# Kernel tuning notes

Measured on AMD Instinct MI355X. Metric: run time of the kernel, lower is better.

Reference implementation:

```python
import jax, jax.numpy as jnp
import numpy as np

B, C, H, W = 8, 256, 64, 64
CQK = C // 8


def setup_inputs() -> dict:
    key = jax.random.key(0)
    ks = jax.random.split(key, 9)
    s_in = 1.0 / np.sqrt(C)
    return {
        "feature1": jax.random.normal(ks[0], (B, C, H, W), jnp.float32),
        "feature2": jax.random.normal(ks[1], (B, C, H, W), jnp.float32),
        "feature3": jax.random.normal(ks[2], (B, C, H, W), jnp.float32),
        # 1x1 conv weights stored as [out_ch, in_ch]
        "wq": jax.random.uniform(ks[3], (CQK, C), jnp.float32, -s_in, s_in),
        "bq": jax.random.uniform(ks[4], (CQK,), jnp.float32, -s_in, s_in),
        "wk": jax.random.uniform(ks[5], (CQK, C), jnp.float32, -s_in, s_in),
        "bk": jax.random.uniform(ks[6], (CQK,), jnp.float32, -s_in, s_in),
        "wv": jax.random.uniform(ks[7], (C, C), jnp.float32, -s_in, s_in),
        "bv": jax.random.uniform(ks[8], (C,), jnp.float32, -s_in, s_in),
    }


def reference(feature1, feature2, feature3, wq, bq, wk, bk, wv, bv):
    b, c, h, w = feature1.shape
    hw = h * w
    # 1x1 convs == per-pixel channel GEMMs
    q = jnp.einsum('bchw,oc->bohw', feature1, wq) + bq[None, :, None, None]
    k = jnp.einsum('bchw,oc->bohw', feature2, wk) + bk[None, :, None, None]
    v = jnp.einsum('bchw,oc->bohw', feature3, wv) + bv[None, :, None, None]
    q = q.reshape(b, -1, hw).transpose(0, 2, 1)  # [b, hw, cqk]
    k = k.reshape(b, -1, hw)                      # [b, cqk, hw]
    v = v.reshape(b, -1, hw)                      # [b, c, hw]
    attn = jax.nn.softmax(jnp.einsum('bnc,bcm->bnm', q, k), axis=-1)  # [b, hw, hw]
    # fused = value @ attn^T  -> [b, c, hw]
    fused = jnp.einsum('bcm,bnm->bcn', v, attn)
    return fused.reshape(b, c, h, w)
```

## Files before the change

### kernel.cpp

```cpp
#include <hip/hip_runtime.h>
#include <math.h>

#define BATCH 8
#define CH    256
#define HWPIX 4096
#define CQK_  32

typedef __bf16 bf16x8 __attribute__((ext_vector_type(8)));
typedef __bf16 bf16x4 __attribute__((ext_vector_type(4)));
typedef __bf16 bf16x2 __attribute__((ext_vector_type(2)));
typedef float  f32x4  __attribute__((ext_vector_type(4)));

#define FS_STR 68

static __device__ inline bf16x8 ld_frag(const __bf16* p) {
  bf16x4 lo = *(const bf16x4*)p;
  bf16x4 hi = *(const bf16x4*)(p + 4);
  return __builtin_shufflevector(lo, hi, 0, 1, 2, 3, 4, 5, 6, 7);
}

static __device__ inline bf16x8 w_frag(const float* p) {
  const float4 a = *(const float4*)p;
  const float4 b = *(const float4*)(p + 4);
  bf16x8 r;
  r[0] = (__bf16)a.x; r[1] = (__bf16)a.y; r[2] = (__bf16)a.z; r[3] = (__bf16)a.w;
  r[4] = (__bf16)b.x; r[5] = (__bf16)b.y; r[6] = (__bf16)b.z; r[7] = (__bf16)b.w;
  return r;
}

__global__ __launch_bounds__(256) void proj_qk_mfma(
    const float* __restrict__ f, const float* __restrict__ W,
    const float* __restrict__ bias, __bf16* __restrict__ outT)
{
  __shared__ __align__(16) __bf16 f_s[64 * FS_STR];
  const int t    = threadIdx.x;
  const int w    = __builtin_amdgcn_readfirstlane(t >> 6);
  const int lane = t & 63;
  const int q16  = lane & 15;
  const int quad = lane >> 4;
  const int b    = blockIdx.y;
  const int n0   = blockIdx.x * 64;
  const float* fb = f + (size_t)b * CH * HWPIX + n0;

  const float bo0 = bias[q16];
  const float bo1 = bias[16 + q16];

  f32x4 acc[2];
  acc[0] = (f32x4){0.f, 0.f, 0.f, 0.f};
  acc[1] = (f32x4){0.f, 0.f, 0.f, 0.f};

  for (int c0 = 0; c0 < CH; c0 += 64) {
    {
      const int n  = t & 63;
      const int cp = (t >> 6) * 2;
#pragma unroll
      for (int k = 0; k < 8; ++k) {
        const int cin = cp + k * 8;
        bf16x2 pk;
        pk[0] = (__bf16)fb[(size_t)(c0 + cin) * HWPIX + n];
        pk[1] = (__bf16)fb[(size_t)(c0 + cin + 1) * HWPIX + n];
        *(bf16x2*)&f_s[n * FS_STR + cin] = pk;
      }
    }
    __syncthreads();

    bf16x8 af[2];
#pragma unroll
    for (int kh = 0; kh < 2; ++kh)
      af[kh] = ld_frag(&f_s[(16 * w + q16) * FS_STR + 32 * kh + quad * 8]);

#pragma unroll
    for (int ot = 0; ot < 2; ++ot) {
#pragma unroll
      for (int kh = 0; kh < 2; ++kh) {
        const bf16x8 wf =
            w_frag(W + (size_t)(16 * ot + q16) * CH + c0 + 32 * kh + quad * 8);
        acc[ot] = __builtin_amdgcn_mfma_f32_16x16x32_bf16(af[kh], wf, acc[ot], 0, 0, 0);
      }
    }
    __syncthreads();
  }

#pragma unroll
  for (int r = 0; r < 4; ++r) {
    const size_t row = (size_t)b * HWPIX + n0 + 16 * w + quad * 4 + r;
    outT[row * CQK_ + q16]      = (__bf16)(acc[0][r] + bo0);
    outT[row * CQK_ + 16 + q16] = (__bf16)(acc[1][r] + bo1);
  }
}

__global__ __launch_bounds__(256) void proj_v_mfma(
    const float* __restrict__ f, const float* __restrict__ W,
    const float* __restrict__ bias, __bf16* __restrict__ outv)
{
  __shared__ __align__(16) __bf16 f_s[64 * FS_STR];
  const int t     = threadIdx.x;
  const int w     = __builtin_amdgcn_readfirstlane(t >> 6);
  const int lane  = t & 63;
  const int q16   = lane & 15;
  const int quad  = lane >> 4;
  const int b     = blockIdx.z;
  const int n0    = blockIdx.x * 64;
  const int cbase = blockIdx.y * 64;
  const float* fb = f + (size_t)b * CH * HWPIX + n0;
  const int crow  = cbase + 16 * w + q16;

  f32x4 acc[4];
#pragma unroll
  for (int nt = 0; nt < 4; ++nt) acc[nt] = (f32x4){0.f, 0.f, 0.f, 0.f};

  for (int c0 = 0; c0 < CH; c0 += 64) {
    {
      const int n  = t & 63;
      const int cp = (t >> 6) * 2;
#pragma unroll
      for (int k = 0; k < 8; ++k) {
        const int cin = cp + k * 8;
        bf16x2 pk;
        pk[0] = (__bf16)fb[(size_t)(c0 + cin) * HWPIX + n];
        pk[1] = (__bf16)fb[(size_t)(c0 + cin + 1) * HWPIX + n];
        *(bf16x2*)&f_s[n * FS_STR + cin] = pk;
      }
    }
    __syncthreads();

    bf16x8 af[2];
#pragma unroll
    for (int kh = 0; kh < 2; ++kh)
      af[kh] = w_frag(W + (size_t)crow * CH + c0 + 32 * kh + quad * 8);

#pragma unroll
    for (int nt = 0; nt < 4; ++nt) {
#pragma unroll
      for (int kh = 0; kh < 2; ++kh) {
        const bf16x8 bfr = ld_frag(&f_s[(16 * nt + q16) * FS_STR + 32 * kh + quad * 8]);
        acc[nt] = __builtin_amdgcn_mfma_f32_16x16x32_bf16(af[kh], bfr, acc[nt], 0, 0, 0);
      }
    }
    __syncthreads();
  }

  const float4 bi = *(const float4*)&bias[cbase + 16 * w + quad * 4];
#pragma unroll
  for (int nt = 0; nt < 4; ++nt) {
#pragma unroll
    for (int r = 0; r < 4; ++r) {
      const int c = cbase + 16 * w + quad * 4 + r;
      outv[((size_t)b * CH + c) * HWPIX + n0 + 16 * nt + q16] =
          (__bf16)(acc[nt][r] + ((const float*)&bi)[r]);
    }
  }
}

__global__ __launch_bounds__(256, 2) void attn_kernel(
    const __bf16* __restrict__ qT, const __bf16* __restrict__ kT,
    const __bf16* __restrict__ vv, float* __restrict__ out)
{
  __shared__ __align__(16) __bf16 p_s[64 * 72];
  __shared__ float L_s[64];

  const int t    = threadIdx.x;
  const int w    = __builtin_amdgcn_readfirstlane(t >> 6);
  const int lane = t & 63;
  const int q16  = lane & 15;
  const int quad = lane >> 4;

  const int b  = blockIdx.x & 7;
  const int q0 = (blockIdx.x >> 3) * 64;

  const __bf16* kTb = kT + (size_t)b * HWPIX * CQK_;
  const __bf16* vbp = vv + ((size_t)b * CH + 64 * w) * HWPIX;

  const bf16x8 qfrag =
      *(const bf16x8*)(qT + ((size_t)b * HWPIX + q0 + 16 * w + q16) * CQK_ + quad * 8);

  f32x4 oacc[4][4];
#pragma unroll
  for (int i = 0; i < 4; ++i)
#pragma unroll
    for (int j = 0; j < 4; ++j)
      oacc[i][j] = (f32x4){0.f, 0.f, 0.f, 0.f};
  float Lp[4] = {0.f, 0.f, 0.f, 0.f};

  bf16x8 kf[4];
#pragma unroll
  for (int mt = 0; mt < 4; ++mt)
    kf[mt] = *(const bf16x8*)(kTb + (size_t)(16 * mt + q16) * CQK_ + quad * 8);

  for (int m0 = 0; m0 < HWPIX; m0 += 64) {
    f32x4 S[4];
#pragma unroll
    for (int mt = 0; mt < 4; ++mt)
      S[mt] = __builtin_amdgcn_mfma_f32_16x16x32_bf16(
          qfrag, kf[mt], (f32x4){0.f, 0.f, 0.f, 0.f}, 0, 0, 0);

    bf16x8 vf[4][2];
#pragma unroll
    for (int ct = 0; ct < 4; ++ct)
#pragma unroll
      for (int mh = 0; mh < 2; ++mh)
        vf[ct][mh] = *(const bf16x8*)(vbp + (size_t)(16 * ct + q16) * HWPIX
                                      + m0 + 32 * mh + quad * 8);

#pragma unroll
    for (int mt = 0; mt < 4; ++mt) {
#pragma unroll
      for (int r = 0; r < 4; ++r) {
        const float e = __expf(S[mt][r]);
        Lp[r] += e;
        p_s[(16 * w + quad * 4 + r) * 72 + 16 * mt + q16] = (__bf16)e;
      }
    }
    __syncthreads();

    const int mn = (m0 + 64) & (HWPIX - 1);
#pragma unroll
    for (int mt = 0; mt < 4; ++mt)
      kf[mt] = *(const bf16x8*)(kTb + (size_t)(mn + 16 * mt + q16) * CQK_ + quad * 8);

    bf16x8 pf[4][2];
#pragma unroll
    for (int nt = 0; nt < 4; ++nt)
#pragma unroll
      for (int mh = 0; mh < 2; ++mh)
        pf[nt][mh] = *(const bf16x8*)(&p_s[(16 * nt + q16) * 72 + 32 * mh + quad * 8]);

#pragma unroll
    for (int ct = 0; ct < 4; ++ct)
#pragma unroll
      for (int nt = 0; nt < 4; ++nt)
#pragma unroll
        for (int mh = 0; mh < 2; ++mh)
          oacc[ct][nt] = __builtin_amdgcn_mfma_f32_16x16x32_bf16(
              vf[ct][mh], pf[nt][mh], oacc[ct][nt], 0, 0, 0);
    __syncthreads();
  }

#pragma unroll
  for (int r = 0; r < 4; ++r) {
    Lp[r] += __shfl_xor(Lp[r], 1);
    Lp[r] += __shfl_xor(Lp[r], 2);
    Lp[r] += __shfl_xor(Lp[r], 4);
    Lp[r] += __shfl_xor(Lp[r], 8);
  }
  if (q16 == 0) {
#pragma unroll
    for (int r = 0; r < 4; ++r) L_s[16 * w + quad * 4 + r] = Lp[r];
  }
  __syncthreads();

  float rinv[4];
#pragma unroll
  for (int nt = 0; nt < 4; ++nt) rinv[nt] = 1.0f / L_s[16 * nt + q16];

  float* ob = out + ((size_t)b * CH + 64 * w) * HWPIX + q0;
#pragma unroll
  for (int ct = 0; ct < 4; ++ct)
#pragma unroll
    for (int r = 0; r < 4; ++r)
#pragma unroll
      for (int nt = 0; nt < 4; ++nt)
        ob[(size_t)(16 * ct + quad * 4 + r) * HWPIX + 16 * nt + q16] =
            oacc[ct][nt][r] * rinv[nt];
}

extern "C" void kernel_launch(void* const* d_in, const int* in_sizes, int n_in,
                              void* d_out, int out_size, void* d_ws, size_t ws_size,
                              hipStream_t stream)
{
  const float* f1 = (const float*)d_in[0];
  const float* f2 = (const float*)d_in[1];
  const float* f3 = (const float*)d_in[2];
  const float* wq = (const float*)d_in[3];
  const float* bq = (const float*)d_in[4];
  const float* wk = (const float*)d_in[5];
  const float* bk = (const float*)d_in[6];
  const float* wv = (const float*)d_in[7];
  const float* bv = (const float*)d_in[8];
  float* outp = (float*)d_out;

  __bf16* qTw = (__bf16*)d_ws;
  __bf16* kTw = qTw + (size_t)BATCH * HWPIX * CQK_;
  __bf16* vw  = kTw + (size_t)BATCH * HWPIX * CQK_;

  proj_qk_mfma<<<dim3(64, 8), 256, 0, stream>>>(f1, wq, bq, qTw);
  proj_qk_mfma<<<dim3(64, 8), 256, 0, stream>>>(f2, wk, bk, kTw);
  proj_v_mfma <<<dim3(64, 4, 8), 256, 0, stream>>>(f3, wv, bv, vw);
  attn_kernel <<<dim3(512), 256, 0, stream>>>(qTw, kTw, vw, outp);
}
```

Baseline: 319.0 us.

## Merge projection kernels and software-pipeline attention with double-buffered P tiles

The three projection launches become one kernel: Q and K are computed together, V is split into two 128-channel halves per block, and staging uses float4 loads. The attention loop double-buffers the probability tile in shared memory, so the QK^T MFMAs and exp for the next key tile overlap with the PV MFMAs of the current one, and K fragments are prefetched two tiles ahead. The aim is to cut launch overhead and exposed latency, at the cost of more LDS and registers per block, which may lower occupancy.

```diff
diff --git a/kernel.cpp b/kernel.cpp
--- a/kernel.cpp
+++ b/kernel.cpp
@@ -28,135 +28,138 @@
   return r;
 }
 
-__global__ __launch_bounds__(256) void proj_qk_mfma(
-    const float* __restrict__ f, const float* __restrict__ W,
-    const float* __restrict__ bias, __bf16* __restrict__ outT)
+__global__ __launch_bounds__(256, 4) void proj_all(
+    const float* __restrict__ f1, const float* __restrict__ f2,
+    const float* __restrict__ f3,
+    const float* __restrict__ wq, const float* __restrict__ bq,
+    const float* __restrict__ wk, const float* __restrict__ bk,
+    const float* __restrict__ wv, const float* __restrict__ bv,
+    __bf16* __restrict__ qT, __bf16* __restrict__ kT, __bf16* __restrict__ vv)
 {
-  __shared__ __align__(16) __bf16 f_s[64 * FS_STR];
+  __shared__ __align__(16) __bf16 f_s[2][64 * FS_STR];
   const int t    = threadIdx.x;
   const int w    = __builtin_amdgcn_readfirstlane(t >> 6);
   const int lane = t & 63;
   const int q16  = lane & 15;
   const int quad = lane >> 4;
-  const int b    = blockIdx.y;
+  const int b    = blockIdx.z;
   const int n0   = blockIdx.x * 64;
-  const float* fb = f + (size_t)b * CH * HWPIX + n0;
-
-  const float bo0 = bias[q16];
-  const float bo1 = bias[16 + q16];
-
-  f32x4 acc[2];
-  acc[0] = (f32x4){0.f, 0.f, 0.f, 0.f};
-  acc[1] = (f32x4){0.f, 0.f, 0.f, 0.f};
-
-  for (int c0 = 0; c0 < CH; c0 += 64) {
-    {
-      const int n  = t & 63;
-      const int cp = (t >> 6) * 2;
-#pragma unroll
-      for (int k = 0; k < 8; ++k) {
-        const int cin = cp + k * 8;
-        bf16x2 pk;
-        pk[0] = (__bf16)fb[(size_t)(c0 + cin) * HWPIX + n];
-        pk[1] = (__bf16)fb[(size_t)(c0 + cin + 1) * HWPIX + n];
-        *(bf16x2*)&f_s[n * FS_STR + cin] = pk;
-      }
-    }
-    __syncthreads();
-
-    bf16x8 af[2];
-#pragma unroll
-    for (int kh = 0; kh < 2; ++kh)
-      af[kh] = ld_frag(&f_s[(16 * w + q16) * FS_STR + 32 * kh + quad * 8]);
-
-#pragma unroll
-    for (int ot = 0; ot < 2; ++ot) {
+  const int mode = blockIdx.y;
+
+  const int sn  = (t & 15) * 4;
+  const int scp = (t >> 4) * 2;
+#define STAGE(fb, c0, dst)                                                      \
+  {                                                                             \
+    _Pragma("unroll") for (int rr = 0; rr < 2; ++rr) {                          \
+      const int c = rr * 32 + scp;                                              \
+      const float4 a0 = *(const float4*)&(fb)[(size_t)((c0) + c) * HWPIX + sn]; \
+      const float4 a1 = *(const float4*)&(fb)[(size_t)((c0) + c + 1) * HWPIX + sn]; \
+      _Pragma("unroll") for (int i = 0; i < 4; ++i) {                           \
+        bf16x2 pk;                                                              \
+        pk[0] = (__bf16)((const float*)&a0)[i];                                 \
+        pk[1] = (__bf16)((const float*)&a1)[i];                                 \
+        *(bf16x2*)&(dst)[(sn + i) * FS_STR + c] = pk;                           \
+      }                                                                         \
+    }                                                                           \
+  }
+
+  if (mode == 0) {
+    const float* f1b = f1 + (size_t)b * CH * HWPIX + n0;
+    const float* f2b = f2 + (size_t)b * CH * HWPIX + n0;
+    f32x4 accQ[2], accK[2];
+#pragma unroll
+    for (int i = 0; i < 2; ++i) {
+      accQ[i] = (f32x4){0.f, 0.f, 0.f, 0.f};
+      accK[i] = (f32x4){0.f, 0.f, 0.f, 0.f};
+    }
+    for (int c0 = 0; c0 < CH; c0 += 64) {
+      STAGE(f1b, c0, f_s[0]);
+      STAGE(f2b, c0, f_s[1]);
+      __syncthreads();
+      bf16x8 afQ[2], afK[2];
 #pragma unroll
       for (int kh = 0; kh < 2; ++kh) {
-        const bf16x8 wf =
-            w_frag(W + (size_t)(16 * ot + q16) * CH + c0 + 32 * kh + quad * 8);
-        acc[ot] = __builtin_amdgcn_mfma_f32_16x16x32_bf16(af[kh], wf, acc[ot], 0, 0, 0);
-      }
-    }
-    __syncthreads();
-  }
-
-#pragma unroll
-  for (int r = 0; r < 4; ++r) {
-    const size_t row = (size_t)b * HWPIX + n0 + 16 * w + quad * 4 + r;
-    outT[row * CQK_ + q16]      = (__bf16)(acc[0][r] + bo0);
-    outT[row * CQK_ + 16 + q16] = (__bf16)(acc[1][r] + bo1);
-  }
-}
-
-__global__ __launch_bounds__(256) void proj_v_mfma(
-    const float* __restrict__ f, const float* __restrict__ W,
-    const float* __restrict__ bias, __bf16* __restrict__ outv)
-{
-  __shared__ __align__(16) __bf16 f_s[64 * FS_STR];
-  const int t     = threadIdx.x;
-  const int w     = __builtin_amdgcn_readfirstlane(t >> 6);
-  const int lane  = t & 63;
-  const int q16   = lane & 15;
-  const int quad  = lane >> 4;
-  const int b     = blockIdx.z;
-  const int n0    = blockIdx.x * 64;
-  const int cbase = blockIdx.y * 64;
-  const float* fb = f + (size_t)b * CH * HWPIX + n0;
-  const int crow  = cbase + 16 * w + q16;
-
-  f32x4 acc[4];
-#pragma unroll
-  for (int nt = 0; nt < 4; ++nt) acc[nt] = (f32x4){0.f, 0.f, 0.f, 0.f};
-
-  for (int c0 = 0; c0 < CH; c0 += 64) {
-    {
-      const int n  = t & 63;
-      const int cp = (t >> 6) * 2;
-#pragma unroll
-      for (int k = 0; k < 8; ++k) {
-        const int cin = cp + k * 8;
-        bf16x2 pk;
-        pk[0] = (__bf16)fb[(size_t)(c0 + cin) * HWPIX + n];
-        pk[1] = (__bf16)fb[(size_t)(c0 + cin + 1) * HWPIX + n];
-        *(bf16x2*)&f_s[n * FS_STR + cin] = pk;
-      }
-    }
-    __syncthreads();
-
-    bf16x8 af[2];
-#pragma unroll
-    for (int kh = 0; kh < 2; ++kh)
-      af[kh] = w_frag(W + (size_t)crow * CH + c0 + 32 * kh + quad * 8);
-
-#pragma unroll
-    for (int nt = 0; nt < 4; ++nt) {
-#pragma unroll
-      for (int kh = 0; kh < 2; ++kh) {
-        const bf16x8 bfr = ld_frag(&f_s[(16 * nt + q16) * FS_STR + 32 * kh + quad * 8]);
-        acc[nt] = __builtin_amdgcn_mfma_f32_16x16x32_bf16(af[kh], bfr, acc[nt], 0, 0, 0);
-      }
-    }
-    __syncthreads();
-  }
-
-  const float4 bi = *(const float4*)&bias[cbase + 16 * w + quad * 4];
-#pragma unroll
-  for (int nt = 0; nt < 4; ++nt) {
+        afQ[kh] = ld_frag(&f_s[0][(16 * w + q16) * FS_STR + 32 * kh + quad * 8]);
+        afK[kh] = ld_frag(&f_s[1][(16 * w + q16) * FS_STR + 32 * kh + quad * 8]);
+      }
+#pragma unroll
+      for (int ot = 0; ot < 2; ++ot) {
+#pragma unroll
+        for (int kh = 0; kh < 2; ++kh) {
+          const bf16x8 wfq =
+              w_frag(wq + (size_t)(16 * ot + q16) * CH + c0 + 32 * kh + quad * 8);
+          accQ[ot] = __builtin_amdgcn_mfma_f32_16x16x32_bf16(afQ[kh], wfq, accQ[ot], 0, 0, 0);
+          const bf16x8 wfk =
+              w_frag(wk + (size_t)(16 * ot + q16) * CH + c0 + 32 * kh + quad * 8);
+          accK[ot] = __builtin_amdgcn_mfma_f32_16x16x32_bf16(afK[kh], wfk, accK[ot], 0, 0, 0);
+        }
+      }
+      __syncthreads();
+    }
+    const float bq0 = bq[q16], bq1 = bq[16 + q16];
+    const float bk0 = bk[q16], bk1 = bk[16 + q16];
 #pragma unroll
     for (int r = 0; r < 4; ++r) {
-      const int c = cbase + 16 * w + quad * 4 + r;
-      outv[((size_t)b * CH + c) * HWPIX + n0 + 16 * nt + q16] =
-          (__bf16)(acc[nt][r] + ((const float*)&bi)[r]);
-    }
-  }
+      const size_t row = (size_t)b * HWPIX + n0 + 16 * w + quad * 4 + r;
+      qT[row * CQK_ + q16]      = (__bf16)(accQ[0][r] + bq0);
+      qT[row * CQK_ + 16 + q16] = (__bf16)(accQ[1][r] + bq1);
+      kT[row * CQK_ + q16]      = (__bf16)(accK[0][r] + bk0);
+      kT[row * CQK_ + 16 + q16] = (__bf16)(accK[1][r] + bk1);
+    }
+  } else {
+    const int cbase = (mode - 1) * 128;
+    const float* f3b = f3 + (size_t)b * CH * HWPIX + n0;
+    f32x4 acc[2][4];
+#pragma unroll
+    for (int ct = 0; ct < 2; ++ct)
+#pragma unroll
+      for (int nt = 0; nt < 4; ++nt) acc[ct][nt] = (f32x4){0.f, 0.f, 0.f, 0.f};
+
+    for (int c0 = 0; c0 < CH; c0 += 64) {
+      STAGE(f3b, c0, f_s[0]);
+      __syncthreads();
+      bf16x8 af[2][2];
+#pragma unroll
+      for (int ct = 0; ct < 2; ++ct)
+#pragma unroll
+        for (int kh = 0; kh < 2; ++kh)
+          af[ct][kh] = w_frag(wv + (size_t)(cbase + 64 * ct + 16 * w + q16) * CH
+                              + c0 + 32 * kh + quad * 8);
+#pragma unroll
+      for (int nt = 0; nt < 4; ++nt) {
+#pragma unroll
+        for (int kh = 0; kh < 2; ++kh) {
+          const bf16x8 bfr = ld_frag(&f_s[0][(16 * nt + q16) * FS_STR + 32 * kh + quad * 8]);
+#pragma unroll
+          for (int ct = 0; ct < 2; ++ct)
+            acc[ct][nt] = __builtin_amdgcn_mfma_f32_16x16x32_bf16(
+                af[ct][kh], bfr, acc[ct][nt], 0, 0, 0);
+        }
+      }
+      __syncthreads();
+    }
+#pragma unroll
+    for (int ct = 0; ct < 2; ++ct) {
+      const float4 bi = *(const float4*)&bv[cbase + 64 * ct + 16 * w + quad * 4];
+#pragma unroll
+      for (int nt = 0; nt < 4; ++nt) {
+#pragma unroll
+        for (int r = 0; r < 4; ++r) {
+          const int c = cbase + 64 * ct + 16 * w + quad * 4 + r;
+          vv[((size_t)b * CH + c) * HWPIX + n0 + 16 * nt + q16] =
+              (__bf16)(acc[ct][nt][r] + ((const float*)&bi)[r]);
+        }
+      }
+    }
+  }
+#undef STAGE
 }
 
 __global__ __launch_bounds__(256, 2) void attn_kernel(
     const __bf16* __restrict__ qT, const __bf16* __restrict__ kT,
     const __bf16* __restrict__ vv, float* __restrict__ out)
 {
-  __shared__ __align__(16) __bf16 p_s[64 * 72];
+  __shared__ __align__(16) __bf16 p_s[2][64 * 72];
   __shared__ float L_s[64];
 
   const int t    = threadIdx.x;
@@ -169,7 +172,12 @@
   const int q0 = (blockIdx.x >> 3) * 64;
 
   const __bf16* kTb = kT + (size_t)b * HWPIX * CQK_;
-  const __bf16* vbp = vv + ((size_t)b * CH + 64 * w) * HWPIX;
+  const int koff = q16 * CQK_ + quad * 8;
+
+  const __bf16* vp[4];
+#pragma unroll
+  for (int ct = 0; ct < 4; ++ct)
+    vp[ct] = vv + ((size_t)b * CH + 64 * w + 16 * ct + q16) * HWPIX + quad * 8;
 
   const bf16x8 qfrag =
       *(const bf16x8*)(qT + ((size_t)b * HWPIX + q0 + 16 * w + q16) * CQK_ + quad * 8);
@@ -185,45 +193,66 @@
   bf16x8 kf[4];
 #pragma unroll
   for (int mt = 0; mt < 4; ++mt)
-    kf[mt] = *(const bf16x8*)(kTb + (size_t)(16 * mt + q16) * CQK_ + quad * 8);
-
-  for (int m0 = 0; m0 < HWPIX; m0 += 64) {
-    f32x4 S[4];
+    kf[mt] = *(const bf16x8*)(kTb + koff + mt * 512);
+  {
+    f32x4 Sv[4];
 #pragma unroll
     for (int mt = 0; mt < 4; ++mt)
-      S[mt] = __builtin_amdgcn_mfma_f32_16x16x32_bf16(
+      Sv[mt] = __builtin_amdgcn_mfma_f32_16x16x32_bf16(
           qfrag, kf[mt], (f32x4){0.f, 0.f, 0.f, 0.f}, 0, 0, 0);
-
+    const __bf16* kb1 = kTb + 64 * CQK_;
+#pragma unroll
+    for (int mt = 0; mt < 4; ++mt)
+      kf[mt] = *(const bf16x8*)(kb1 + koff + mt * 512);
+#pragma unroll
+    for (int mt = 0; mt < 4; ++mt) {
+#pragma unroll
+      for (int r = 0; r < 4; ++r) {
+        const float e = __expf(Sv[mt][r]);
+        Lp[r] += e;
+        p_s[0][(16 * w + quad * 4 + r) * 72 + 16 * mt + q16] = (__bf16)e;
+      }
+    }
+  }
+  __syncthreads();
+
+  for (int i = 0; i < 64; ++i) {
     bf16x8 vf[4][2];
 #pragma unroll
     for (int ct = 0; ct < 4; ++ct)
 #pragma unroll
       for (int mh = 0; mh < 2; ++mh)
-        vf[ct][mh] = *(const bf16x8*)(vbp + (size_t)(16 * ct + q16) * HWPIX
-                                      + m0 + 32 * mh + quad * 8);
-
-#pragma unroll
-    for (int mt = 0; mt < 4; ++mt) {
-#pragma unroll
-      for (int r = 0; r < 4; ++r) {
-        const float e = __expf(S[mt][r]);
-        Lp[r] += e;
-        p_s[(16 * w + quad * 4 + r) * 72 + 16 * mt + q16] = (__bf16)e;
-      }
-    }
-    __syncthreads();
-
-    const int mn = (m0 + 64) & (HWPIX - 1);
-#pragma unroll
-    for (int mt = 0; mt < 4; ++mt)
-      kf[mt] = *(const bf16x8*)(kTb + (size_t)(mn + 16 * mt + q16) * CQK_ + quad * 8);
-
+        vf[ct][mh] = *(const bf16x8*)(vp[ct] + mh * 32);
+
+    const __bf16* pb = p_s[i & 1];
     bf16x8 pf[4][2];
 #pragma unroll
     for (int nt = 0; nt < 4; ++nt)
 #pragma unroll
       for (int mh = 0; mh < 2; ++mh)
-        pf[nt][mh] = *(const bf16x8*)(&p_s[(16 * nt + q16) * 72 + 32 * mh + quad * 8]);
+        pf[nt][mh] = *(const bf16x8*)(&pb[(16 * nt + q16) * 72 + 32 * mh + quad * 8]);
+
+    if (i < 63) {
+      f32x4 Sv[4];
+#pragma unroll
+      for (int mt = 0; mt < 4; ++mt)
+        Sv[mt] = __builtin_amdgcn_mfma_f32_16x16x32_bf16(
+            qfrag, kf[mt], (f32x4){0.f, 0.f, 0.f, 0.f}, 0, 0, 0);
+      const __bf16* kb2 = kTb + (size_t)((i + 2) & 63) * (64 * CQK_);
+#pragma unroll
+      for (int mt = 0; mt < 4; ++mt)
+        kf[mt] = *(const bf16x8*)(kb2 + koff + mt * 512);
+      __bf16* pw = p_s[(i + 1) & 1];
+#pragma unroll
+      for (int mt = 0; mt < 4; ++mt) {
+#pragma unroll
+        for (int r = 0; r < 4; ++r) {
+          const float e = __expf(Sv[mt][r]);
+          Lp[r] += e;
+          pw[(16 * w + quad * 4 + r) * 72 + 16 * mt + q16] = (__bf16)e;
+        }
+      }
+    }
 
 #pragma unroll
     for (int ct = 0; ct < 4; ++ct)
@@ -233,6 +262,9 @@
         for (int mh = 0; mh < 2; ++mh)
           oacc[ct][nt] = __builtin_amdgcn_mfma_f32_16x16x32_bf16(
               vf[ct][mh], pf[nt][mh], oacc[ct][nt], 0, 0, 0);
+
+#pragma unroll
+    for (int ct = 0; ct < 4; ++ct) vp[ct] += 64;
     __syncthreads();
   }
 
@@ -283,8 +315,7 @@
   __bf16* kTw = qTw + (size_t)BATCH * HWPIX * CQK_;
   __bf16* vw  = kTw + (size_t)BATCH * HWPIX * CQK_;
 
-  proj_qk_mfma<<<dim3(64, 8), 256, 0, stream>>>(f1, wq, bq, qTw);
-  proj_qk_mfma<<<dim3(64, 8), 256, 0, stream>>>(f2, wk, bk, kTw);
-  proj_v_mfma <<<dim3(64, 4, 8), 256, 0, stream>>>(f3, wv, bv, vw);
-  attn_kernel <<<dim3(512), 256, 0, stream>>>(qTw, kTw, vw, outp);
-}
+  proj_all<<<dim3(64, 3, 8), 256, 0, stream>>>(f1, f2, f3, wq, bq, wk, bk, wv, bv,
+                                               qTw, kTw, vw);
+  attn_kernel<<<dim3(512), 256, 0, stream>>>(qTw, kTw, vw, outp);
+}
```

Result: no change. 314.3 us (-1.5%).
